# Performance work log

Measured on AMD Instinct MI355X. Metric: run time of the kernel, lower is better.

The kernel has to match this reference:

```python
import jax, jax.numpy as jnp
import numpy as np

N_NODES = 50000
N_EDGES = 500000
NODE_DIM = 128
EDGE_DIM = 128
HIDDEN = 256


def setup_inputs() -> dict:
    key = jax.random.key(0)
    k1, k2, k3, k4, k5 = jax.random.split(key, 5)
    node_features = jax.random.normal(k1, (N_NODES, NODE_DIM), dtype=jnp.float32)
    edge_features = jax.random.normal(k2, (N_EDGES, EDGE_DIM), dtype=jnp.float32)
    edge_index = jax.random.randint(k3, (2, N_EDGES), 0, N_NODES, dtype=jnp.int64)
    in_dim = 2 * NODE_DIM + EDGE_DIM
    W1 = jax.random.normal(k4, (in_dim, HIDDEN), dtype=jnp.float32) * (1.0 / np.sqrt(in_dim))
    b1 = jnp.zeros((HIDDEN,), dtype=jnp.float32)
    W2 = jax.random.normal(k5, (HIDDEN, EDGE_DIM), dtype=jnp.float32) * (1.0 / np.sqrt(HIDDEN))
    b2 = jnp.zeros((EDGE_DIM,), dtype=jnp.float32)
    return {"node_features": node_features, "edge_features": edge_features,
            "edge_index": edge_index, "W1": W1, "b1": b1, "W2": W2, "b2": b2}


def reference(node_features, edge_features, edge_index, W1, b1, W2, b2):
    # h_edge' = h_edge + MLP(concat(h_src, h_dst, h_edge)); dropout is identity (eval)
    src, dst = edge_index[0], edge_index[1]
    h_src = node_features[src]                    # (E, node_dim)
    h_dst = node_features[dst]                    # (E, node_dim)
    combined = jnp.concatenate([h_src, h_dst, edge_features], axis=1)  # (E, 2*nd+ed)
    h = jax.nn.relu(combined @ W1 + b1)           # (E, hidden)
    update = h @ W2 + b2                          # (E, edge_dim)
    return edge_features + update
```

## Files before the change

### kernel.cpp

```cpp
#include <hip/hip_runtime.h>

#define E_TOTAL   500000
#define NN        50000
#define ND        128
#define ED        128
#define HID       256
#define IND       384
#define EB        64
#define NBLOCKS   ((E_TOTAL + EB - 1) / EB)

typedef float  f32x4  __attribute__((ext_vector_type(4)));
typedef short  bf16x8 __attribute__((ext_vector_type(8)));

__device__ __forceinline__ unsigned short f2bf(float f) {
    unsigned int u = __float_as_uint(f);
    u += 0x7FFFu + ((u >> 16) & 1u);
    return (unsigned short)(u >> 16);
}
__device__ __forceinline__ float bf2f(unsigned short h) {
    return __uint_as_float(((unsigned int)h) << 16);
}

__global__ void prep_w1(const float* __restrict__ w1, unsigned short* __restrict__ w1t) {
    int i = blockIdx.x * blockDim.x + threadIdx.x;
    if (i >= IND * HID) return;
    int k = i / HID, n = i % HID;
    w1t[n * IND + k] = f2bf(w1[i]);
}

__global__ void prep_w2(const float* __restrict__ w2, unsigned short* __restrict__ w2t) {
    int i = blockIdx.x * blockDim.x + threadIdx.x;
    if (i >= HID * ED) return;
    int k = i / ED, n = i % ED;
    w2t[n * HID + k] = f2bf(w2[i]);
}

__global__ __launch_bounds__(256, 2)
void prep_ptab(const float* __restrict__ nf,
               const unsigned short* __restrict__ w1t,
               const float* __restrict__ b1,
               unsigned short* __restrict__ Psrc,
               unsigned short* __restrict__ Pdst) {
    __shared__ unsigned short An[EB * ND];
    const int tid  = threadIdx.x;
    const int base = blockIdx.x * EB;
    const int lane = tid & 63;
    const int w    = tid >> 6;
    const int l15  = lane & 15;
    const int lhi  = lane >> 4;

    #pragma unroll
    for (int it = 0; it < 4; ++it) {
        int item = tid + it * 256;
        int row = item >> 4, cc = item & 15;
        int nidx = base + row;
        if (nidx >= NN) nidx = NN - 1;
        const float* p = nf + (size_t)nidx * ND + cc * 8;
        float4 f0 = *(const float4*)p;
        float4 f1 = *(const float4*)(p + 4);
        bf16x8 val;
        val[0] = (short)f2bf(f0.x); val[1] = (short)f2bf(f0.y);
        val[2] = (short)f2bf(f0.z); val[3] = (short)f2bf(f0.w);
        val[4] = (short)f2bf(f1.x); val[5] = (short)f2bf(f1.y);
        val[6] = (short)f2bf(f1.z); val[7] = (short)f2bf(f1.w);
        *(bf16x8*)(An + row * ND + ((cc * 8) ^ ((row & 7) * 8))) = val;
    }
    __syncthreads();

    f32x4 accs[4][4], accd[4][4];
    #pragma unroll
    for (int mt = 0; mt < 4; ++mt)
        #pragma unroll
        for (int nt = 0; nt < 4; ++nt) { accs[mt][nt] = (f32x4)0.0f; accd[mt][nt] = (f32x4)0.0f; }

    #pragma unroll
    for (int ks = 0; ks < 4; ++ks) {
        int c0 = ks * 32 + lhi * 8;
        bf16x8 a[4];
        #pragma unroll
        for (int mt = 0; mt < 4; ++mt) {
            int row = mt * 16 + l15;
            a[mt] = *(const bf16x8*)(An + row * ND + (c0 ^ ((row & 7) * 8)));
        }
        #pragma unroll
        for (int nt = 0; nt < 4; ++nt) {
            int n = w * 64 + nt * 16 + l15;
            bf16x8 bs = *(const bf16x8*)(w1t + (size_t)n * IND + c0);
            bf16x8 bd = *(const bf16x8*)(w1t + (size_t)n * IND + 128 + c0);
            #pragma unroll
            for (int mt = 0; mt < 4; ++mt) {
                accs[mt][nt] = __builtin_amdgcn_mfma_f32_16x16x32_bf16(a[mt], bs, accs[mt][nt], 0, 0, 0);
                accd[mt][nt] = __builtin_amdgcn_mfma_f32_16x16x32_bf16(a[mt], bd, accd[mt][nt], 0, 0, 0);
            }
        }
    }

    #pragma unroll
    for (int nt = 0; nt < 4; ++nt) {
        int col = w * 64 + nt * 16 + l15;
        float bias = b1[col];
        #pragma unroll
        for (int mt = 0; mt < 4; ++mt) {
            #pragma unroll
            for (int r = 0; r < 4; ++r) {
                int row = mt * 16 + lhi * 4 + r;
                int nidx = base + row;
                if (nidx < NN) {
                    size_t off = (size_t)nidx * HID + col;
                    Psrc[off] = f2bf(accs[mt][nt][r] + bias);
                    Pdst[off] = f2bf(accd[mt][nt][r]);
                }
            }
        }
    }
}

__global__ __launch_bounds__(256, 3)
void edge_mlp(const float* __restrict__ edgef,
              const int* __restrict__ eidx,
              const unsigned short* __restrict__ Psrc,
              const unsigned short* __restrict__ Pdst,
              const unsigned short* __restrict__ w1t,
              const unsigned short* __restrict__ w2t,
              const float* __restrict__ b2,
              float* __restrict__ out) {
    __shared__ unsigned short Ae[EB * ND];
    __shared__ unsigned short Hs[EB * HID];

    const int tid  = threadIdx.x;
    const int base = blockIdx.x * EB;
    const int lane = tid & 63;
    const int w    = tid >> 6;
    const int l15  = lane & 15;
    const int lhi  = lane >> 4;
    const int* srcI = eidx;
    const int* dstI = eidx + E_TOTAL;

    #pragma unroll
    for (int it = 0; it < 4; ++it) {
        int item = tid + it * 256;
        int row = item >> 4, cc = item & 15;
        int e = base + row;
        int el = e < E_TOTAL ? e : E_TOTAL - 1;
        const float* p = edgef + (size_t)el * ED + cc * 8;
        float4 f0 = *(const float4*)p;
        float4 f1 = *(const float4*)(p + 4);
        bf16x8 val;
        val[0] = (short)f2bf(f0.x); val[1] = (short)f2bf(f0.y);
        val[2] = (short)f2bf(f0.z); val[3] = (short)f2bf(f0.w);
        val[4] = (short)f2bf(f1.x); val[5] = (short)f2bf(f1.y);
        val[6] = (short)f2bf(f1.z); val[7] = (short)f2bf(f1.w);
        *(bf16x8*)(Ae + row * ND + ((cc * 8) ^ ((row & 7) * 8))) = val;
    }

    #pragma unroll
    for (int it = 0; it < 8; ++it) {
        int item = tid + it * 256;
        int row = item >> 5, cc = item & 31;
        int e = base + row;
        int el = e < E_TOTAL ? e : E_TOTAL - 1;
        int s = srcI[el], d = dstI[el];
        bf16x8 vs = *(const bf16x8*)(Psrc + (size_t)s * HID + cc * 8);
        bf16x8 vd = *(const bf16x8*)(Pdst + (size_t)d * HID + cc * 8);
        bf16x8 o;
        #pragma unroll
        for (int j = 0; j < 8; ++j)
            o[j] = (short)f2bf(bf2f((unsigned short)vs[j]) + bf2f((unsigned short)vd[j]));
        *(bf16x8*)(Hs + row * HID + ((cc * 8) ^ ((row & 7) * 8))) = o;
    }
    __syncthreads();

    f32x4 acc1[4][4];
    #pragma unroll
    for (int mt = 0; mt < 4; ++mt)
        #pragma unroll
        for (int nt = 0; nt < 4; ++nt)
            acc1[mt][nt] = (f32x4)0.0f;

    #pragma unroll
    for (int ks = 0; ks < 4; ++ks) {
        int c0 = ks * 32 + lhi * 8;
        bf16x8 a[4];
        #pragma unroll
        for (int mt = 0; mt < 4; ++mt) {
            int row = mt * 16 + l15;
            a[mt] = *(const bf16x8*)(Ae + row * ND + (c0 ^ ((row & 7) * 8)));
        }
        #pragma unroll
        for (int nt = 0; nt < 4; ++nt) {
            int n = w * 64 + nt * 16 + l15;
            bf16x8 b = *(const bf16x8*)(w1t + (size_t)n * IND + 256 + c0);
            #pragma unroll
            for (int mt = 0; mt < 4; ++mt)
                acc1[mt][nt] = __builtin_amdgcn_mfma_f32_16x16x32_bf16(a[mt], b, acc1[mt][nt], 0, 0, 0);
        }
    }

    #pragma unroll
    for (int nt = 0; nt < 4; ++nt) {
        int col = w * 64 + nt * 16 + l15;
        #pragma unroll
        for (int mt = 0; mt < 4; ++mt) {
            #pragma unroll
            for (int r = 0; r < 4; ++r) {
                int row = mt * 16 + lhi * 4 + r;
                int idx = row * HID + (col ^ ((row & 7) * 8));
                float v = acc1[mt][nt][r] + bf2f(Hs[idx]);
                v = v > 0.0f ? v : 0.0f;
                Hs[idx] = f2bf(v);
            }
        }
    }
    __syncthreads();

    f32x4 acc2[4][2];
    #pragma unroll
    for (int mt = 0; mt < 4; ++mt)
        #pragma unroll
        for (int nt = 0; nt < 2; ++nt)
            acc2[mt][nt] = (f32x4)0.0f;

    #pragma unroll
    for (int ks = 0; ks < 8; ++ks) {
        int c0 = ks * 32 + lhi * 8;
        bf16x8 a[4];
        #pragma unroll
        for (int mt = 0; mt < 4; ++mt) {
            int row = mt * 16 + l15;
            a[mt] = *(const bf16x8*)(Hs + row * HID + (c0 ^ ((row & 7) * 8)));
        }
        #pragma unroll
        for (int nt = 0; nt < 2; ++nt) {
            int n = w * 32 + nt * 16 + l15;
            bf16x8 b = *(const bf16x8*)(w2t + (size_t)n * HID + c0);
            #pragma unroll
            for (int mt = 0; mt < 4; ++mt)
                acc2[mt][nt] = __builtin_amdgcn_mfma_f32_16x16x32_bf16(a[mt], b, acc2[mt][nt], 0, 0, 0);
        }
    }

    #pragma unroll
    for (int nt = 0; nt < 2; ++nt) {
        int col = w * 32 + nt * 16 + l15;
        float bias = b2[col];
        #pragma unroll
        for (int mt = 0; mt < 4; ++mt) {
            #pragma unroll
            for (int r = 0; r < 4; ++r) {
                int row = mt * 16 + lhi * 4 + r;
                int e = base + row;
                if (e < E_TOTAL) {
                    float ev = bf2f(Ae[row * ND + (col ^ ((row & 7) * 8))]);
                    out[(size_t)e * ED + col] = ev + acc2[mt][nt][r] + bias;
                }
            }
        }
    }
}

extern "C" void kernel_launch(void* const* d_in, const int* in_sizes, int n_in,
                              void* d_out, int out_size, void* d_ws, size_t ws_size,
                              hipStream_t stream) {
    const float* nf   = (const float*)d_in[0];
    const float* ef   = (const float*)d_in[1];
    const int*   eidx = (const int*)d_in[2];
    const float* W1   = (const float*)d_in[3];
    const float* b1   = (const float*)d_in[4];
    const float* W2   = (const float*)d_in[5];
    const float* b2   = (const float*)d_in[6];
    float* out = (float*)d_out;

    unsigned short* w1t  = (unsigned short*)d_ws;
    unsigned short* w2t  = w1t + IND * HID;
    unsigned short* Psrc = w2t + HID * ED;
    unsigned short* Pdst = Psrc + (size_t)NN * HID;

    prep_w1<<<(IND * HID + 255) / 256, 256, 0, stream>>>(W1, w1t);
    prep_w2<<<(HID * ED + 255) / 256, 256, 0, stream>>>(W2, w2t);
    prep_ptab<<<(NN + EB - 1) / EB, 256, 0, stream>>>(nf, w1t, b1, Psrc, Pdst);
    edge_mlp<<<NBLOCKS, 256, 0, stream>>>(ef, eidx, Psrc, Pdst, w1t, w2t, b2, out);
}
```

Measured before the change: 289.6 us.

## Make edge MLP blocks persistent over tiles with register-prefetched gathers

Each edge_mlp block now processes four 64-edge tiles. The gathers of Psrc/Pdst rows and edge features for the next tile are issued into registers before the current tile's MFMA work, then written to shared memory once the current tile is finished, so global load latency overlaps compute. The two weight-prep kernels are also merged into one launch. The prefetch buffers add a lot of register pressure, which together with launch_bounds(256,3) may cause spills or lower occupancy, and the grid shrinks by a factor of four.

```diff
diff --git a/kernel.cpp b/kernel.cpp
--- a/kernel.cpp
+++ b/kernel.cpp
@@ -7,7 +7,8 @@
 #define HID       256
 #define IND       384
 #define EB        64
-#define NBLOCKS   ((E_TOTAL + EB - 1) / EB)
+#define TPB       4
+#define NBLOCKS   ((E_TOTAL + EB * TPB - 1) / (EB * TPB))
 
 typedef float  f32x4  __attribute__((ext_vector_type(4)));
 typedef short  bf16x8 __attribute__((ext_vector_type(8)));
@@ -21,18 +22,17 @@
     return __uint_as_float(((unsigned int)h) << 16);
 }
 
-__global__ void prep_w1(const float* __restrict__ w1, unsigned short* __restrict__ w1t) {
+__global__ void prep_weights(const float* __restrict__ w1, const float* __restrict__ w2,
+                             unsigned short* __restrict__ w1t, unsigned short* __restrict__ w2t) {
     int i = blockIdx.x * blockDim.x + threadIdx.x;
-    if (i >= IND * HID) return;
-    int k = i / HID, n = i % HID;
-    w1t[n * IND + k] = f2bf(w1[i]);
-}
-
-__global__ void prep_w2(const float* __restrict__ w2, unsigned short* __restrict__ w2t) {
-    int i = blockIdx.x * blockDim.x + threadIdx.x;
-    if (i >= HID * ED) return;
-    int k = i / ED, n = i % ED;
-    w2t[n * HID + k] = f2bf(w2[i]);
+    if (i < IND * HID) {
+        int k = i / HID, n = i % HID;
+        w1t[n * IND + k] = f2bf(w1[i]);
+    } else if (i < IND * HID + HID * ED) {
+        int q = i - IND * HID;
+        int k = q / ED, n = q % ED;
+        w2t[n * HID + k] = f2bf(w2[q]);
+    }
 }
 
 __global__ __launch_bounds__(256, 2)
@@ -41,9 +41,9 @@
                const float* __restrict__ b1,
                unsigned short* __restrict__ Psrc,
                unsigned short* __restrict__ Pdst) {
-    __shared__ unsigned short An[EB * ND];
+    __shared__ unsigned short An[64 * ND];
     const int tid  = threadIdx.x;
-    const int base = blockIdx.x * EB;
+    const int base = blockIdx.x * 64;
     const int lane = tid & 63;
     const int w    = tid >> 6;
     const int l15  = lane & 15;
@@ -128,132 +128,164 @@
     __shared__ unsigned short Hs[EB * HID];
 
     const int tid  = threadIdx.x;
-    const int base = blockIdx.x * EB;
     const int lane = tid & 63;
     const int w    = tid >> 6;
     const int l15  = lane & 15;
     const int lhi  = lane >> 4;
     const int* srcI = eidx;
     const int* dstI = eidx + E_TOTAL;
-
-    #pragma unroll
-    for (int it = 0; it < 4; ++it) {
-        int item = tid + it * 256;
-        int row = item >> 4, cc = item & 15;
-        int e = base + row;
-        int el = e < E_TOTAL ? e : E_TOTAL - 1;
-        const float* p = edgef + (size_t)el * ED + cc * 8;
-        float4 f0 = *(const float4*)p;
-        float4 f1 = *(const float4*)(p + 4);
-        bf16x8 val;
-        val[0] = (short)f2bf(f0.x); val[1] = (short)f2bf(f0.y);
-        val[2] = (short)f2bf(f0.z); val[3] = (short)f2bf(f0.w);
-        val[4] = (short)f2bf(f1.x); val[5] = (short)f2bf(f1.y);
-        val[6] = (short)f2bf(f1.z); val[7] = (short)f2bf(f1.w);
-        *(bf16x8*)(Ae + row * ND + ((cc * 8) ^ ((row & 7) * 8))) = val;
-    }
-
-    #pragma unroll
-    for (int it = 0; it < 8; ++it) {
-        int item = tid + it * 256;
-        int row = item >> 5, cc = item & 31;
-        int e = base + row;
-        int el = e < E_TOTAL ? e : E_TOTAL - 1;
-        int s = srcI[el], d = dstI[el];
-        bf16x8 vs = *(const bf16x8*)(Psrc + (size_t)s * HID + cc * 8);
-        bf16x8 vd = *(const bf16x8*)(Pdst + (size_t)d * HID + cc * 8);
-        bf16x8 o;
-        #pragma unroll
-        for (int j = 0; j < 8; ++j)
-            o[j] = (short)f2bf(bf2f((unsigned short)vs[j]) + bf2f((unsigned short)vd[j]));
-        *(bf16x8*)(Hs + row * HID + ((cc * 8) ^ ((row & 7) * 8))) = o;
-    }
+    const int block0 = blockIdx.x * (EB * TPB);
+
+    bf16x8 vs[8], vd[8];
+    float4 ae0[4], ae1[4];
+
+    auto STAGE_ISSUE = [&](int tbase) {
+        #pragma unroll
+        for (int it = 0; it < 8; ++it) {
+            int item = tid + it * 256;
+            int row = item >> 5, cc = item & 31;
+            int e = tbase + row;
+            int el = e < E_TOTAL ? e : E_TOTAL - 1;
+            int s = srcI[el], d = dstI[el];
+            vs[it] = *(const bf16x8*)(Psrc + (size_t)s * HID + cc * 8);
+            vd[it] = *(const bf16x8*)(Pdst + (size_t)d * HID + cc * 8);
+        }
+        #pragma unroll
+        for (int it = 0; it < 4; ++it) {
+            int item = tid + it * 256;
+            int row = item >> 4, cc = item & 15;
+            int e = tbase + row;
+            int el = e < E_TOTAL ? e : E_TOTAL - 1;
+            const float* p = edgef + (size_t)el * ED + cc * 8;
+            ae0[it] = *(const float4*)p;
+            ae1[it] = *(const float4*)(p + 4);
+        }
+    };
+
+    auto STAGE_WRITE = [&]() {
+        #pragma unroll
+        for (int it = 0; it < 8; ++it) {
+            int item = tid + it * 256;
+            int row = item >> 5, cc = item & 31;
+            bf16x8 o;
+            #pragma unroll
+            for (int j = 0; j < 8; ++j)
+                o[j] = (short)f2bf(bf2f((unsigned short)vs[it][j]) + bf2f((unsigned short)vd[it][j]));
+            *(bf16x8*)(Hs + row * HID + ((cc * 8) ^ ((row & 7) * 8))) = o;
+        }
+        #pragma unroll
+        for (int it = 0; it < 4; ++it) {
+            int item = tid + it * 256;
+            int row = item >> 4, cc = item & 15;
+            bf16x8 val;
+            val[0] = (short)f2bf(ae0[it].x); val[1] = (short)f2bf(ae0[it].y);
+            val[2] = (short)f2bf(ae0[it].z); val[3] = (short)f2bf(ae0[it].w);
+            val[4] = (short)f2bf(ae1[it].x); val[5] = (short)f2bf(ae1[it].y);
+            val[6] = (short)f2bf(ae1[it].z); val[7] = (short)f2bf(ae1[it].w);
+            *(bf16x8*)(Ae + row * ND + ((cc * 8) ^ ((row & 7) * 8))) = val;
+        }
+    };
+
+    STAGE_ISSUE(block0);
+    STAGE_WRITE();
     __syncthreads();
 
-    f32x4 acc1[4][4];
-    #pragma unroll
-    for (int mt = 0; mt < 4; ++mt)
-        #pragma unroll
-        for (int nt = 0; nt < 4; ++nt)
-            acc1[mt][nt] = (f32x4)0.0f;
-
-    #pragma unroll
-    for (int ks = 0; ks < 4; ++ks) {
-        int c0 = ks * 32 + lhi * 8;
-        bf16x8 a[4];
-        #pragma unroll
-        for (int mt = 0; mt < 4; ++mt) {
-            int row = mt * 16 + l15;
-            a[mt] = *(const bf16x8*)(Ae + row * ND + (c0 ^ ((row & 7) * 8)));
-        }
+    for (int tp = 0; tp < TPB; ++tp) {
+        const int base = block0 + tp * EB;
+
+        if (tp + 1 < TPB) STAGE_ISSUE(base + EB);
+
+        f32x4 acc1[4][4];
+        #pragma unroll
+        for (int mt = 0; mt < 4; ++mt)
+            #pragma unroll
+            for (int nt = 0; nt < 4; ++nt)
+                acc1[mt][nt] = (f32x4)0.0f;
+
+        #pragma unroll
+        for (int ks = 0; ks < 4; ++ks) {
+            int c0 = ks * 32 + lhi * 8;
+            bf16x8 a[4];
+            #pragma unroll
+            for (int mt = 0; mt < 4; ++mt) {
+                int row = mt * 16 + l15;
+                a[mt] = *(const bf16x8*)(Ae + row * ND + (c0 ^ ((row & 7) * 8)));
+            }
+            #pragma unroll
+            for (int nt = 0; nt < 4; ++nt) {
+                int n = w * 64 + nt * 16 + l15;
+                bf16x8 b = *(const bf16x8*)(w1t + (size_t)n * IND + 256 + c0);
+                #pragma unroll
+                for (int mt = 0; mt < 4; ++mt)
+                    acc1[mt][nt] = __builtin_amdgcn_mfma_f32_16x16x32_bf16(a[mt], b, acc1[mt][nt], 0, 0, 0);
+            }
+        }
+
         #pragma unroll
         for (int nt = 0; nt < 4; ++nt) {
-            int n = w * 64 + nt * 16 + l15;
-            bf16x8 b = *(const bf16x8*)(w1t + (size_t)n * IND + 256 + c0);
-            #pragma unroll
-            for (int mt = 0; mt < 4; ++mt)
-                acc1[mt][nt] = __builtin_amdgcn_mfma_f32_16x16x32_bf16(a[mt], b, acc1[mt][nt], 0, 0, 0);
-        }
-    }
-
-    #pragma unroll
-    for (int nt = 0; nt < 4; ++nt) {
-        int col = w * 64 + nt * 16 + l15;
-        #pragma unroll
-        for (int mt = 0; mt < 4; ++mt) {
-            #pragma unroll
-            for (int r = 0; r < 4; ++r) {
-                int row = mt * 16 + lhi * 4 + r;
-                int idx = row * HID + (col ^ ((row & 7) * 8));
-                float v = acc1[mt][nt][r] + bf2f(Hs[idx]);
-                v = v > 0.0f ? v : 0.0f;
-                Hs[idx] = f2bf(v);
-            }
-        }
-    }
-    __syncthreads();
-
-    f32x4 acc2[4][2];
-    #pragma unroll
-    for (int mt = 0; mt < 4; ++mt)
-        #pragma unroll
-        for (int nt = 0; nt < 2; ++nt)
-            acc2[mt][nt] = (f32x4)0.0f;
-
-    #pragma unroll
-    for (int ks = 0; ks < 8; ++ks) {
-        int c0 = ks * 32 + lhi * 8;
-        bf16x8 a[4];
-        #pragma unroll
-        for (int mt = 0; mt < 4; ++mt) {
-            int row = mt * 16 + l15;
-            a[mt] = *(const bf16x8*)(Hs + row * HID + (c0 ^ ((row & 7) * 8)));
-        }
+            int col = w * 64 + nt * 16 + l15;
+            #pragma unroll
+            for (int mt = 0; mt < 4; ++mt) {
+                #pragma unroll
+                for (int r = 0; r < 4; ++r) {
+                    int row = mt * 16 + lhi * 4 + r;
+                    int idx = row * HID + (col ^ ((row & 7) * 8));
+                    float v = acc1[mt][nt][r] + bf2f(Hs[idx]);
+                    v = v > 0.0f ? v : 0.0f;
+                    Hs[idx] = f2bf(v);
+                }
+            }
+        }
+        __syncthreads();
+
+        f32x4 acc2[4][2];
+        #pragma unroll
+        for (int mt = 0; mt < 4; ++mt)
+            #pragma unroll
+            for (int nt = 0; nt < 2; ++nt)
+                acc2[mt][nt] = (f32x4)0.0f;
+
+        #pragma unroll
+        for (int ks = 0; ks < 8; ++ks) {
+            int c0 = ks * 32 + lhi * 8;
+            bf16x8 a[4];
+            #pragma unroll
+            for (int mt = 0; mt < 4; ++mt) {
+                int row = mt * 16 + l15;
+                a[mt] = *(const bf16x8*)(Hs + row * HID + (c0 ^ ((row & 7) * 8)));
+            }
+            #pragma unroll
+            for (int nt = 0; nt < 2; ++nt) {
+                int n = w * 32 + nt * 16 + l15;
+                bf16x8 b = *(const bf16x8*)(w2t + (size_t)n * HID + c0);
+                #pragma unroll
+                for (int mt = 0; mt < 4; ++mt)
+                    acc2[mt][nt] = __builtin_amdgcn_mfma_f32_16x16x32_bf16(a[mt], b, acc2[mt][nt], 0, 0, 0);
+            }
+        }
+
         #pragma unroll
         for (int nt = 0; nt < 2; ++nt) {
-            int n = w * 32 + nt * 16 + l15;
-            bf16x8 b = *(const bf16x8*)(w2t + (size_t)n * HID + c0);
-            #pragma unroll
-            for (int mt = 0; mt < 4; ++mt)
-                acc2[mt][nt] = __builtin_amdgcn_mfma_f32_16x16x32_bf16(a[mt], b, acc2[mt][nt], 0, 0, 0);
-        }
-    }
-
-    #pragma unroll
-    for (int nt = 0; nt < 2; ++nt) {
-        int col = w * 32 + nt * 16 + l15;
-        float bias = b2[col];
-        #pragma unroll
-        for (int mt = 0; mt < 4; ++mt) {
-            #pragma unroll
-            for (int r = 0; r < 4; ++r) {
-                int row = mt * 16 + lhi * 4 + r;
-                int e = base + row;
-                if (e < E_TOTAL) {
-                    float ev = bf2f(Ae[row * ND + (col ^ ((row & 7) * 8))]);
-                    out[(size_t)e * ED + col] = ev + acc2[mt][nt][r] + bias;
+            int col = w * 32 + nt * 16 + l15;
+            float bias = b2[col];
+            #pragma unroll
+            for (int mt = 0; mt < 4; ++mt) {
+                #pragma unroll
+                for (int r = 0; r < 4; ++r) {
+                    int row = mt * 16 + lhi * 4 + r;
+                    int e = base + row;
+                    if (e < E_TOTAL) {
+                        float ev = bf2f(Ae[row * ND + (col ^ ((row & 7) * 8))]);
+                        out[(size_t)e * ED + col] = ev + acc2[mt][nt][r] + bias;
+                    }
                 }
             }
+        }
+
+        if (tp + 1 < TPB) {
+            __syncthreads();
+            STAGE_WRITE();
+            __syncthreads();
         }
     }
 }
@@ -275,8 +307,8 @@
     unsigned short* Psrc = w2t + HID * ED;
     unsigned short* Pdst = Psrc + (size_t)NN * HID;
 
-    prep_w1<<<(IND * HID + 255) / 256, 256, 0, stream>>>(W1, w1t);
-    prep_w2<<<(HID * ED + 255) / 256, 256, 0, stream>>>(W2, w2t);
-    prep_ptab<<<(NN + EB - 1) / EB, 256, 0, stream>>>(nf, w1t, b1, Psrc, Pdst);
+    int wtotal = IND * HID + HID * ED;
+    prep_weights<<<(wtotal + 255) / 256, 256, 0, stream>>>(W1, W2, w1t, w2t);
+    prep_ptab<<<(NN + 63) / 64, 256, 0, stream>>>(nf, w1t, b1, Psrc, Pdst);
     edge_mlp<<<NBLOCKS, 256, 0, stream>>>(ef, eidx, Psrc, Pdst, w1t, w2t, b2, out);
 }
```

After: 1.073 ms. +270.3%, slower.
